# Kernel tuning notes

Measured on AMD Instinct MI355X. Metric: run time of the kernel, lower is better.

## Reference

```python
import jax, jax.numpy as jnp
import numpy as np

HEADS, K = 8, 7

def setup_inputs() -> dict:
    key = jax.random.key(0)
    ks = jax.random.split(key, 8)
    C = 432
    B, H, W = 1, 56, 56
    n = lambda k, s, std: jax.random.normal(k, s, dtype=jnp.float32) * std
    return {
        "x": n(ks[0], (B, H, W, C), 1.0),
        "qkv_w": n(ks[1], (3 * C, C), 0.02),
        "qkv_b": jnp.zeros((3 * C,), jnp.float32),
        "rpb": n(ks[2], (HEADS, 2 * K - 1, 2 * K - 1), 0.02),
        "conv1_w": n(ks[3], (C, C // 54, K, K), 0.05),   # grouped conv, groups=54 -> 8 in-ch per group
        "conv1_b": jnp.zeros((C,), jnp.float32),
        "conv2_w": n(ks[4], (K * K * HEADS, C, 1, 1), 0.05),
        "conv2_b": jnp.zeros((K * K * HEADS,), jnp.float32),
        "ghost_head": n(ks[5], (C, K, K), 0.02),
        "proj2_w": n(ks[6], (C, 2 * C), 0.02),
        "proj2_b": jnp.zeros((C,), jnp.float32),
    }

def _nat_indices(L, K):
    i = jnp.arange(L)
    ni = jnp.clip(i - K // 2, 0, L - K)                      # clamped window start (NAT semantics)
    idx = ni[:, None] + jnp.arange(K)[None, :]               # [L,K] neighbor coords
    rpb_idx = (K - 1) - (i - ni)[:, None] + jnp.arange(K)[None, :]  # [L,K] rpb lookup
    return idx, rpb_idx

def reference(x, qkv_w, qkv_b, rpb, conv1_w, conv1_b, conv2_w, conv2_b, ghost_head, proj2_w, proj2_b):
    B, H, W, C = x.shape
    hd = C // HEADS
    scale = hd ** -0.5
    qkv = (x @ qkv_w.T + qkv_b).reshape(B, H, W, 3, HEADS, hd)
    qkv = jnp.transpose(qkv, (3, 0, 4, 1, 2, 5))             # [3,B,heads,H,W,hd]
    q, k, v = qkv[0], qkv[1], qkv[2]
    q = q * scale
    idx_i, rpb_i = _nat_indices(H, K)
    idx_j, rpb_j = _nat_indices(W, K)
    ii = idx_i[:, None, :, None]                             # [H,1,K,1]
    jj = idx_j[None, :, None, :]                             # [1,W,1,K]
    # ---- NAT QK + RPB ----
    k_nbr = k[:, :, ii, jj, :]                               # [B,heads,H,W,K,K,hd]
    attn = jnp.einsum('bghwd,bghwuvd->bghwuv', q, k_nbr)
    bias = rpb[:, rpb_i[:, None, :, None], rpb_j[None, :, None, :]]  # [heads,H,W,K,K]
    attn = (attn + bias[None]).reshape(B, HEADS, H, W, K * K)
    attn = jax.nn.softmax(attn, axis=-1)
    # ---- Hadamard conv-attention branch ----
    to_nchw = lambda t: jnp.transpose(t, (0, 2, 3, 1, 4)).reshape(B, H, W, C).transpose(0, 3, 1, 2)
    had = to_nchw(q) * to_nchw(k) * scale                    # note: q already scaled once (faithful)
    h = jax.lax.conv_general_dilated(had, conv1_w, (1, 1), ((K // 2, K // 2), (K // 2, K // 2)),
                                     feature_group_count=54,
                                     dimension_numbers=('NCHW', 'OIHW', 'NCHW')) + conv1_b[None, :, None, None]
    h = jax.nn.gelu(h, approximate=False)
    h = jax.lax.conv_general_dilated(h, conv2_w, (1, 1), ((0, 0), (0, 0)),
                                     dimension_numbers=('NCHW', 'OIHW', 'NCHW')) + conv2_b[None, :, None, None]
    h = jax.nn.softmax(h, axis=1)                            # softmax over all heads*K*K channels
    h_attn = jnp.transpose(h, (0, 2, 3, 1)).reshape(B, H, W, HEADS, K * K).transpose(0, 3, 1, 2, 4)
    attn_A = jnp.concatenate([attn, h_attn], axis=-1)        # [B,heads,H,W,2*K*K]
    # ---- ELSA ghost-head local aggregation (zero-padded centered window, lam=0, gamma=1) ----
    v_tmp = to_nchw(v)                                       # [B,C,H,W]
    a_tmp = jnp.transpose(attn_A, (0, 2, 3, 1, 4)).reshape(B, H, W, -1).transpose(0, 3, 1, 2)
    G = 2 * HEADS                                            # 2*K*K slots per head -> 2*heads attn groups
    a_g = a_tmp.reshape(B, G, K * K, H, W)
    vp = jnp.pad(v_tmp, ((0, 0), (0, 0), (K // 2, K // 2), (K // 2, K // 2)))
    pi = jnp.arange(H)[:, None] + jnp.arange(K)[None, :]     # [H,K]
    pj = jnp.arange(W)[:, None] + jnp.arange(K)[None, :]
    patches = vp[:, :, pi[:, None, :, None], pj[None, :, None, :]].reshape(B, C, H, W, K * K)
    elsa = jnp.einsum('bgchwk,bgkhw->bgchw',
                      patches.reshape(B, G, C // G, H, W, K * K), a_g).reshape(B, C, H, W)
    elsa = elsa + jnp.einsum('bchwk,ck->bchw', patches, ghost_head.reshape(C, K * K))
    attn_tmp = jnp.transpose(elsa, (0, 2, 3, 1)).reshape(B, H, W, HEADS, hd).transpose(0, 3, 1, 2, 4)
    # ---- NAT AV over fused attention (both 49-slot halves share the NAT neighborhood) ----
    a2 = (attn_A[..., :K * K] + attn_A[..., K * K:]).reshape(B, HEADS, H, W, K, K)
    v_nbr = v[:, :, ii, jj, :]                               # [B,heads,H,W,K,K,hd]
    av = jnp.einsum('bghwuv,bghwuvd->bghwd', a2, v_nbr)
    out = jnp.concatenate([av, attn_tmp], axis=-1)           # [B,heads,H,W,2*hd]
    out = jnp.transpose(out, (0, 2, 3, 1, 4)).reshape(B, H, W, 2 * C)
    return out @ proj2_w.T + proj2_b
```

## Files before the change

kernel.cpp:

```cpp
#include <hip/hip_runtime.h>
#include <hip/hip_bf16.h>
#include <math.h>

#define N_PIX 3136
#define NPAD 3200
#define CDIM 432
#define NHEADS 8
#define HD 54
#define KK 49
#define C2 392

typedef __attribute__((ext_vector_type(8))) short bf16x8;
typedef __attribute__((ext_vector_type(4))) float f32x4;
typedef __attribute__((ext_vector_type(8))) unsigned short ushort8;

__device__ __forceinline__ void gload_lds16(const void* g, void* l) {
    __builtin_amdgcn_global_load_lds(
        (const __attribute__((address_space(1))) void*)g,
        (__attribute__((address_space(3))) void*)l, 16, 0, 0);
}

__device__ __forceinline__ unsigned short f2bf(float f) {
    __hip_bfloat16 b = __float2bfloat16(f);
    unsigned short u;
    __builtin_memcpy(&u, &b, 2);
    return u;
}

__device__ __forceinline__ size_t perm_off(int r, int k, int Kp) {
    int p = ((k >> 3) & 7) ^ (r & 7);
    return (size_t)r * Kp + ((k >> 6) << 6) + (p << 3) + (k & 7);
}

__device__ __forceinline__ void convert_body(
    const float* __restrict__ src, __hip_bfloat16* __restrict__ dst,
    int Mlog, int Mpad, int Klog, int Kp, int id)
{
    int chunks = Kp >> 3;
    if (id >= Mpad * chunks) return;
    int r = id / chunks, cb = id % chunks;
    int k0 = cb << 3;
    __hip_bfloat16 vv[8];
    #pragma unroll
    for (int e = 0; e < 8; e++) {
        int k = k0 + e;
        float f = (r < Mlog && k < Klog) ? src[(size_t)r * Klog + k] : 0.f;
        vv[e] = __float2bfloat16(f);
    }
    int p = (cb & 7) ^ (r & 7);
    __hip_bfloat16* d = dst + (size_t)r * Kp + ((cb >> 3) << 6) + (p << 3);
    *(ushort8*)d = *(const ushort8*)vv;
}

__global__ __launch_bounds__(256) void prep_kernel(
    const float* __restrict__ x, const float* __restrict__ qkv_w,
    const float* __restrict__ conv2_w, const float* __restrict__ proj2_w,
    const float* __restrict__ ghost,
    __hip_bfloat16* __restrict__ xb, __hip_bfloat16* __restrict__ qkvwb,
    __hip_bfloat16* __restrict__ c2wb, __hip_bfloat16* __restrict__ p2wb,
    float* __restrict__ ghostT, __hip_bfloat16* __restrict__ qkzero)
{
    int b = blockIdx.x;
    if (b < 83) {
        int id = b * 256 + threadIdx.x;
        if (id < CDIM * KK) {
            int cc = id / KK, t = id % KK;
            ghostT[t * CDIM + cc] = ghost[id];
        }
    } else if (b < 769) {
        convert_body(x, xb, 3136, 3136, 432, 448, (b - 83) * 256 + threadIdx.x);
    } else if (b < 1063) {
        convert_body(qkv_w, qkvwb, 1296, 1344, 432, 448, (b - 769) * 256 + threadIdx.x);
    } else if (b < 1161) {
        convert_body(conv2_w, c2wb, 392, 448, 432, 448, (b - 1063) * 256 + threadIdx.x);
    } else if (b < 1357) {
        convert_body(proj2_w, p2wb, 432, 448, 864, 896, (b - 1161) * 256 + threadIdx.x);
    } else {
        int id = (b - 1357) * 256 + threadIdx.x;
        if (id < 409600) ((ushort8*)qkzero)[id] = (ushort8)0;
    }
}

__global__ __launch_bounds__(256) void gemm_mfma(
    const __hip_bfloat16* __restrict__ A, const __hip_bfloat16* __restrict__ B,
    const float* __restrict__ bias,
    float* __restrict__ O0, float* __restrict__ O1,
    __hip_bfloat16* __restrict__ VB,
    __hip_bfloat16* __restrict__ QB, __hip_bfloat16* __restrict__ KB,
    int Nlog, int Kp, int mode, float qscale, int ldO)
{
    __shared__ __hip_bfloat16 lA[64 * 64];
    __shared__ __hip_bfloat16 lB[64 * 64];
    const int tid = threadIdx.x;
    const int w = tid >> 6, lane = tid & 63;
    const int row0 = blockIdx.y * 64, col0 = blockIdx.x * 64;
    const int wr = (w >> 1) * 32, wc = (w & 1) * 32;
    const int srow = lane >> 3, schk = lane & 7;
    f32x4 acc[2][2] = {};

    for (int k0 = 0; k0 < Kp; k0 += 64) {
        #pragma unroll
        for (int t = 0; t < 2; t++) {
            int lid = w * 2 + t;
            const __hip_bfloat16* ga =
                A + (size_t)(row0 + lid * 8 + srow) * Kp + k0 + schk * 8;
            gload_lds16(ga, &lA[lid * 8 * 64]);
            const __hip_bfloat16* gb =
                B + (size_t)(col0 + lid * 8 + srow) * Kp + k0 + schk * 8;
            gload_lds16(gb, &lB[lid * 8 * 64]);
        }
        __syncthreads();
        #pragma unroll
        for (int ks = 0; ks < 2; ks++) {
            bf16x8 af[2], bfr[2];
            int c = ks * 4 + (lane >> 4);
            #pragma unroll
            for (int mi = 0; mi < 2; mi++) {
                int ra = wr + mi * 16 + (lane & 15);
                af[mi] = *(const bf16x8*)&lA[ra * 64 + ((c ^ (ra & 7)) << 3)];
                int rb = wc + mi * 16 + (lane & 15);
                bfr[mi] = *(const bf16x8*)&lB[rb * 64 + ((c ^ (rb & 7)) << 3)];
            }
            #pragma unroll
            for (int mi = 0; mi < 2; mi++)
                #pragma unroll
                for (int ni = 0; ni < 2; ni++)
                    acc[mi][ni] = __builtin_amdgcn_mfma_f32_16x16x32_bf16(
                        af[mi], bfr[ni], acc[mi][ni], 0, 0, 0);
        }
        __syncthreads();
    }

    #pragma unroll
    for (int mi = 0; mi < 2; mi++) {
        #pragma unroll
        for (int ni = 0; ni < 2; ni++) {
            #pragma unroll
            for (int rr = 0; rr < 4; rr++) {
                int r = row0 + wr + mi * 16 + (lane >> 4) * 4 + rr;
                int cc = col0 + wc + ni * 16 + (lane & 15);
                if (cc >= Nlog) continue;
                float val = acc[mi][ni][rr] + bias[cc];
                if (mode == 0) {
                    int s = cc / CDIM, cch = cc - s * CDIM;
                    int hh = cch / HD, dd = cch - hh * HD;
                    if (s == 0) {
                        float qv = val * qscale;
                        O0[(size_t)r * CDIM + cch] = qv;
                        QB[((size_t)hh * NPAD + r) * 64 + dd] = __float2bfloat16(qv);
                    } else if (s == 1) {
                        O1[(size_t)r * CDIM + cch] = val;
                        KB[((size_t)hh * NPAD + r) * 64 + dd] = __float2bfloat16(val);
                    } else {
                        VB[((size_t)hh * N_PIX + r) * 64 + dd] = __float2bfloat16(val);
                    }
                } else {
                    O0[(size_t)r * ldO + cc] = val;
                }
            }
        }
    }
}

__global__ __launch_bounds__(256) void attn_mfma(
    const __hip_bfloat16* __restrict__ qb, const __hip_bfloat16* __restrict__ kb,
    const float* __restrict__ rpb, float* __restrict__ attn)
{
    __shared__ float Sl[16][404];
    __shared__ float rpb_l[169];
    int bid = blockIdx.x;
    int nb = (bid & 7) * 56 + (bid >> 3);
    int h = nb / 56, i = nb - (nb / 56) * 56;
    int tid = threadIdx.x;
    int w = tid >> 6, lane = tid & 63;
    int l15 = lane & 15, l4 = lane >> 4;
    int ni = min(max(i - 3, 0), 49);

    for (int f = tid; f < 169; f += 256) rpb_l[f] = rpb[h * 169 + f];
    __syncthreads();

    const __hip_bfloat16* qrow = qb + ((size_t)h * NPAD + i * 56) * 64;
    const __hip_bfloat16* kwin = kb + ((size_t)h * NPAD + ni * 56) * 64;

    for (int rt = 0; rt < 4; rt++) {
        bf16x8 af0 = *(const bf16x8*)(qrow + (size_t)(rt * 16 + l15) * 64 + l4 * 8);
        bf16x8 af1 = *(const bf16x8*)(qrow + (size_t)(rt * 16 + l15) * 64 + 32 + l4 * 8);
        for (int ct = w; ct < 25; ct += 4) {
            bf16x8 b0 = *(const bf16x8*)(kwin + (size_t)(ct * 16 + l15) * 64 + l4 * 8);
            bf16x8 b1 = *(const bf16x8*)(kwin + (size_t)(ct * 16 + l15) * 64 + 32 + l4 * 8);
            f32x4 acc = {};
            acc = __builtin_amdgcn_mfma_f32_16x16x32_bf16(af0, b0, acc, 0, 0, 0);
            acc = __builtin_amdgcn_mfma_f32_16x16x32_bf16(af1, b1, acc, 0, 0, 0);
            int col = ct * 16 + l15;
            #pragma unroll
            for (int r = 0; r < 4; r++)
                Sl[l4 * 4 + r][col] = acc[r];
        }
        __syncthreads();
        #pragma unroll
        for (int pp = 0; pp < 4; pp++) {
            int j = rt * 16 + w * 4 + pp;
            if (j < 56) {
                int n = i * 56 + j;
                int nj = min(max(j - 3, 0), 49);
                int t = lane;
                float logit = -1e30f;
                if (t < KK) {
                    int u = t / 7, v = t - (t / 7) * 7;
                    int col = u * 56 + nj + v;
                    int ri = 6 - (i - ni) + u;
                    int rj = 6 - (j - nj) + v;
                    logit = Sl[j - rt * 16][col] + rpb_l[ri * 13 + rj];
                }
                float m = logit;
                #pragma unroll
                for (int off = 32; off; off >>= 1) m = fmaxf(m, __shfl_xor(m, off));
                float e = (t < KK) ? expf(logit - m) : 0.f;
                float ssum = e;
                #pragma unroll
                for (int off = 32; off; off >>= 1) ssum += __shfl_xor(ssum, off);
                if (t < KK) attn[(size_t)n * C2 + h * KK + t] = e / ssum;
            }
        }
        __syncthreads();
    }
}

#define TH 4
__global__ __launch_bounds__(256) void conv1_gelu_v2(
    const float* __restrict__ q, const float* __restrict__ k,
    const float* __restrict__ w, const float* __restrict__ b,
    __hip_bfloat16* __restrict__ out, float scale)
{
    int g = blockIdx.x % 54;
    int rt = blockIdx.x / 54;
    int r0 = rt * TH;
    int tid = threadIdx.x;
    int waveid = tid >> 6, lane = tid & 63;
    int ic = lane >> 3, oc = lane & 7;

    __shared__ float smem[10][8][68];

    float* sflat = &smem[0][0][0];
    for (int i = tid; i < 10 * 8 * 68; i += 256) sflat[i] = 0.f;

    float wreg[49];
    {
        const float* wp = w + ((size_t)(g * 8 + oc) * 8 + ic) * 49;
        #pragma unroll
        for (int t = 0; t < 49; t++) wreg[t] = wp[t];
    }
    __syncthreads();

    {
        int lic = tid & 7;
        int lpj = (tid >> 3) & 31;
        for (int rr = 0; rr < 10; rr++) {
            int pi = r0 - 3 + rr;
            if (pi < 0 || pi >= 56) continue;
            #pragma unroll
            for (int p0 = 0; p0 < 56; p0 += 32) {
                int pj = p0 + lpj;
                if (pj < 56) {
                    size_t off = (size_t)(pi * 56 + pj) * CDIM + g * 8 + lic;
                    smem[rr][lic][pj + 3] = q[off] * k[off] * scale;
                }
            }
        }
    }
    __syncthreads();

    int r = r0 + waveid;
    float bias_o = b[g * 8 + oc];
    for (int j0 = 0; j0 < 56; j0 += 4) {
        float acc0 = 0.f, acc1 = 0.f, acc2 = 0.f, acc3 = 0.f;
        #pragma unroll
        for (int u = 0; u < 7; u++) {
            const float* rp = &smem[waveid + u][ic][j0];
            float4 c0 = *(const float4*)(rp);
            float4 c1 = *(const float4*)(rp + 4);
            float4 c2 = *(const float4*)(rp + 8);
            float col[12] = {c0.x, c0.y, c0.z, c0.w,
                             c1.x, c1.y, c1.z, c1.w,
                             c2.x, c2.y, c2.z, c2.w};
            #pragma unroll
            for (int v = 0; v < 7; v++) {
                float wv = wreg[u * 7 + v];
                acc0 += wv * col[v + 0];
                acc1 += wv * col[v + 1];
                acc2 += wv * col[v + 2];
                acc3 += wv * col[v + 3];
            }
        }
        float accs[4] = {acc0, acc1, acc2, acc3};
        #pragma unroll
        for (int jj = 0; jj < 4; jj++) {
            float s = accs[jj];
            s += __shfl_xor(s, 8);
            s += __shfl_xor(s, 16);
            s += __shfl_xor(s, 32);
            accs[jj] = s;
        }
        if (ic == 0) {
            #pragma unroll
            for (int jj = 0; jj < 4; jj++) {
                float a = accs[jj] + bias_o;
                float gl = 0.5f * a * (1.0f + erff(a * 0.70710678118654752f));
                int n = r * 56 + j0 + jj;
                int kch = g * 8 + oc;
                out[perm_off(n, kch, 448)] = __float2bfloat16(gl);
            }
        }
    }
}

__global__ __launch_bounds__(128) void softmax_pack(
    const float* __restrict__ h2, const float* __restrict__ attn,
    unsigned* __restrict__ pk)
{
    __shared__ float red[128];
    int n = blockIdx.x, tid = threadIdx.x;
    const float* row = h2 + (size_t)n * C2;
    float m = -1e30f;
    float rv[4];
    #pragma unroll
    for (int idx = 0; idx < 4; idx++) {
        int c = tid + idx * 128;
        rv[idx] = (c < C2) ? row[c] : -1e30f;
        m = fmaxf(m, rv[idx]);
    }
    red[tid] = m; __syncthreads();
    for (int s = 64; s; s >>= 1) {
        if (tid < s) red[tid] = fmaxf(red[tid], red[tid + s]);
        __syncthreads();
    }
    m = red[0]; __syncthreads();
    float loc = 0.f;
    #pragma unroll
    for (int idx = 0; idx < 4; idx++) {
        int c = tid + idx * 128;
        if (c < C2) { rv[idx] = expf(rv[idx] - m); loc += rv[idx]; }
    }
    red[tid] = loc; __syncthreads();
    for (int s = 64; s; s >>= 1) {
        if (tid < s) red[tid] += red[tid + s];
        __syncthreads();
    }
    float inv = 1.0f / red[0];
    #pragma unroll
    for (int idx = 0; idx < 4; idx++) {
        int c = tid + idx * 128;
        if (c < C2) {
            float hval = rv[idx] * inv;
            float a = attn[(size_t)n * C2 + c];
            int hh = c / KK, t = c - hh * KK;
            unsigned word = ((unsigned)f2bf(a) << 16) | (unsigned)f2bf(a + hval);
            pk[((size_t)n * 8 + hh) * 52 + t] = word;
        }
    }
}

__global__ __launch_bounds__(256) void combine_int(
    const __hip_bfloat16* __restrict__ vb, const unsigned* __restrict__ pk,
    const float* __restrict__ ghostT, __hip_bfloat16* __restrict__ comb)
{
    __shared__ float gs[KK * HD];
    int bid = blockIdx.x;
    int nb = (bid & 7) * 625 + (bid >> 3);
    int h = (nb * 4) / 2500;
    for (int f = threadIdx.x; f < KK * HD; f += 256) {
        int t = f / HD, dd = f - t * HD;
        gs[f] = ghostT[t * CDIM + h * HD + dd];
    }
    __syncthreads();

    int task = nb * 4 + (threadIdx.x >> 6);
    task = __builtin_amdgcn_readfirstlane(task);
    int lane = threadIdx.x & 63;
    int rem = task - h * 2500;
    int i = 3 + rem / 50;
    int j = 3 + (rem - (rem / 50) * 50);
    int n = i * 56 + j;
    int d = (lane < HD) ? lane : (HD - 1);
    bool lo = (d < 27);

    const unsigned* pkrow = pk + ((size_t)n * 8 + h) * 52;
    const __hip_bfloat16* vwin =
        vb + ((size_t)h * N_PIX + (i - 3) * 56 + (j - 3)) * 64 + d;

    float S_ah = 0.f, S_a = 0.f, S_g = 0.f;
    #pragma unroll
    for (int u = 0; u < 7; u++) {
        float vrow[7];
        #pragma unroll
        for (int vv = 0; vv < 7; vv++)
            vrow[vv] = __bfloat162float(vwin[(u * 56 + vv) * 64]);
        #pragma unroll
        for (int vv = 0; vv < 7; vv++) {
            const int t = u * 7 + vv;
            unsigned s = pkrow[t];
            float a  = __uint_as_float(s & 0xFFFF0000u);
            float ah = __uint_as_float(s << 16);
            float gt = gs[t * HD + d];
            S_ah += ah * vrow[vv];
            S_a  += a  * vrow[vv];
            S_g  += gt * vrow[vv];
        }
    }
    if (lane < HD) {
        float av = S_ah;
        float Sh = S_ah - S_a;
        float elsa = S_g + (lo ? S_a : Sh);
        comb[perm_off(n, h * 108 + d, 896)]      = __float2bfloat16(av);
        comb[perm_off(n, h * 108 + 54 + d, 896)] = __float2bfloat16(elsa);
    }
}

__global__ __launch_bounds__(256) void combine_bdr(
    const __hip_bfloat16* __restrict__ vb, const unsigned* __restrict__ pk,
    const float* __restrict__ ghostT, __hip_bfloat16* __restrict__ comb)
{
    __shared__ float gs[KK * HD];
    int bid = blockIdx.x;
    int nb = (bid & 7) * 159 + (bid >> 3);
    int h = (nb * 4) / 636;
    for (int f = threadIdx.x; f < KK * HD; f += 256) {
        int t = f / HD, dd = f - t * HD;
        gs[f] = ghostT[t * CDIM + h * HD + dd];
    }
    __syncthreads();

    int task = nb * 4 + (threadIdx.x >> 6);
    task = __builtin_amdgcn_readfirstlane(task);
    int lane = threadIdx.x & 63;
    int idx = task - h * 636;
    int i, j;
    if (idx < 336) {
        int r = idx / 56;
        i = (r < 3) ? r : 50 + r;
        j = idx - r * 56;
    } else {
        int idx2 = idx - 336;
        i = 3 + idx2 / 6;
        int jj = idx2 - (idx2 / 6) * 6;
        j = (jj < 3) ? jj : 50 + jj;
    }
    int n = i * 56 + j;
    int d = (lane < HD) ? lane : (HD - 1);
    bool lo = (d < 27);

    const unsigned* pkrow = pk + ((size_t)n * 8 + h) * 52;
    int ni = min(max(i - 3, 0), 49), nj = min(max(j - 3, 0), 49);
    const __hip_bfloat16* vhead = vb + (size_t)h * N_PIX * 64 + d;
    const __hip_bfloat16* vbc = vhead + (size_t)(ni * 56 + nj) * 64;

    float S_ahc = 0.f, S_ap = 0.f, S_ahp = 0.f, S_gp = 0.f;
    #pragma unroll
    for (int t = 0; t < KK; t++) {
        const int u = t / 7, vv = t % 7;
        unsigned s = pkrow[t];
        float a  = __uint_as_float(s & 0xFFFF0000u);
        float ah = __uint_as_float(s << 16);
        float vc = __bfloat162float(vbc[(u * 56 + vv) * 64]);
        S_ahc += ah * vc;
        int pi = i + u - 3, pj = j + vv - 3;
        if (pi >= 0 && pi < 56 && pj >= 0 && pj < 56) {
            float vp = __bfloat162float(vhead[(size_t)(pi * 56 + pj) * 64]);
            float gt = gs[t * HD + d];
            S_ahp += ah * vp; S_ap += a * vp; S_gp += gt * vp;
        }
    }
    if (lane < HD) {
        float av = S_ahc;
        float Shp = S_ahp - S_ap;
        float elsa = S_gp + (lo ? S_ap : Shp);
        comb[perm_off(n, h * 108 + d, 896)]      = __float2bfloat16(av);
        comb[perm_off(n, h * 108 + 54 + d, 896)] = __float2bfloat16(elsa);
    }
}

extern "C" void kernel_launch(void* const* d_in, const int* in_sizes, int n_in,
                              void* d_out, int out_size, void* d_ws, size_t ws_size,
                              hipStream_t stream)
{
    const float* x       = (const float*)d_in[0];
    const float* qkv_w   = (const float*)d_in[1];
    const float* qkv_b   = (const float*)d_in[2];
    const float* rpb     = (const float*)d_in[3];
    const float* conv1_w = (const float*)d_in[4];
    const float* conv1_b = (const float*)d_in[5];
    const float* conv2_w = (const float*)d_in[6];
    const float* conv2_b = (const float*)d_in[7];
    const float* ghost   = (const float*)d_in[8];
    const float* proj2_w = (const float*)d_in[9];
    const float* proj2_b = (const float*)d_in[10];
    float* out = (float*)d_out;

    float* ws = (float*)d_ws;
    const size_t NC = (size_t)N_PIX * CDIM;
    const size_t NA = (size_t)N_PIX * C2;
    float* q      = ws;
    float* k      = q + NC;
    float* attn   = k + NC;
    float* hat    = attn + NA;
    float* ghostT = hat + NA;
    unsigned* pk  = (unsigned*)(ghostT + 21168);
    __hip_bfloat16* bfbase = (__hip_bfloat16*)(pk + 1304576);
    __hip_bfloat16* xb     = bfbase;
    __hip_bfloat16* qkvwb  = xb    + (size_t)3136 * 448;
    __hip_bfloat16* c2wb   = qkvwb + (size_t)1344 * 448;
    __hip_bfloat16* p2wb   = c2wb  + (size_t)448 * 448;
    __hip_bfloat16* hb     = p2wb  + (size_t)448 * 896;
    __hip_bfloat16* cb     = hb    + (size_t)3136 * 448;
    __hip_bfloat16* vb16   = cb    + (size_t)3136 * 896;
    __hip_bfloat16* qb16   = vb16  + (size_t)8 * N_PIX * 64;
    __hip_bfloat16* kb16   = qb16  + (size_t)8 * NPAD * 64;

    const float scale = 0.13608276348795434f;

    prep_kernel<<<2957, 256, 0, stream>>>(
        x, qkv_w, conv2_w, proj2_w, ghost, xb, qkvwb, c2wb, p2wb, ghostT, qb16);

    gemm_mfma<<<dim3(21, 49), 256, 0, stream>>>(
        xb, qkvwb, qkv_b, q, k, vb16, qb16, kb16, 1296, 448, 0, scale, 0);

    attn_mfma<<<448, 256, 0, stream>>>(qb16, kb16, rpb, attn);

    conv1_gelu_v2<<<54 * 14, 256, 0, stream>>>(q, k, conv1_w, conv1_b, hb, scale);

    gemm_mfma<<<dim3(7, 49), 256, 0, stream>>>(
        hb, c2wb, conv2_b, hat, nullptr, nullptr, nullptr, nullptr,
        392, 448, 1, 1.f, 392);

    softmax_pack<<<N_PIX, 128, 0, stream>>>(hat, attn, pk);

    combine_int<<<5000, 256, 0, stream>>>(vb16, pk, ghostT, cb);
    combine_bdr<<<1272, 256, 0, stream>>>(vb16, pk, ghostT, cb);

    gemm_mfma<<<dim3(7, 49), 256, 0, stream>>>(
        cb, p2wb, proj2_b, out, nullptr, nullptr, nullptr, nullptr,
        432, 896, 1, 1.f, 432);
}
```

Measured before the change: 151.2 us.

## Use 128x128 GEMM tiles, zero only Q/K pad columns, vectorize conv staging

The MFMA GEMM tile is raised from 64x64 to 128x128 per block. Each wave now computes a 64x64 sub-tile with 4x4 accumulators, and a row bound check is added for the M edge. The prep kernel no longer zeroes the whole bf16 Q/K buffers; it clears only the padding head-dim columns 54..63, which shrinks its grid. The conv1 staging loop switches to float4 loads of q and k. The larger tiles cut global and LDS traffic per FLOP, but the conv2 and proj GEMMs drop to about 100 blocks, which can leave CUs idle. Edge tiles also read past logical rows into neighbouring buffers.

```diff
diff --git a/kernel.cpp b/kernel.cpp
--- a/kernel.cpp
+++ b/kernel.cpp
@@ -13,6 +13,7 @@
 typedef __attribute__((ext_vector_type(8))) short bf16x8;
 typedef __attribute__((ext_vector_type(4))) float f32x4;
 typedef __attribute__((ext_vector_type(8))) unsigned short ushort8;
+typedef __attribute__((ext_vector_type(2))) unsigned short ushort2v;
 
 __device__ __forceinline__ void gload_lds16(const void* g, void* l) {
     __builtin_amdgcn_global_load_lds(
@@ -58,7 +59,7 @@
     const float* __restrict__ ghost,
     __hip_bfloat16* __restrict__ xb, __hip_bfloat16* __restrict__ qkvwb,
     __hip_bfloat16* __restrict__ c2wb, __hip_bfloat16* __restrict__ p2wb,
-    float* __restrict__ ghostT, __hip_bfloat16* __restrict__ qkzero)
+    float* __restrict__ ghostT, __hip_bfloat16* __restrict__ qkbase)
 {
     int b = blockIdx.x;
     if (b < 83) {
@@ -77,31 +78,35 @@
         convert_body(proj2_w, p2wb, 432, 448, 864, 896, (b - 1161) * 256 + threadIdx.x);
     } else {
         int id = (b - 1357) * 256 + threadIdx.x;
-        if (id < 409600) ((ushort8*)qkzero)[id] = (ushort8)0;
-    }
-}
-
-__global__ __launch_bounds__(256) void gemm_mfma(
+        if (id < 2 * 8 * NPAD) {
+            __hip_bfloat16* p = qkbase + (size_t)id * 64;
+            *(ushort2v*)((unsigned short*)p + 54) = (ushort2v)0;
+            *(ushort8*)((unsigned short*)p + 56) = (ushort8)0;
+        }
+    }
+}
+
+__global__ __launch_bounds__(256) void gemm_mfma2(
     const __hip_bfloat16* __restrict__ A, const __hip_bfloat16* __restrict__ B,
     const float* __restrict__ bias,
     float* __restrict__ O0, float* __restrict__ O1,
     __hip_bfloat16* __restrict__ VB,
     __hip_bfloat16* __restrict__ QB, __hip_bfloat16* __restrict__ KB,
-    int Nlog, int Kp, int mode, float qscale, int ldO)
-{
-    __shared__ __hip_bfloat16 lA[64 * 64];
-    __shared__ __hip_bfloat16 lB[64 * 64];
+    int Mlog, int Nlog, int Kp, int mode, float qscale, int ldO)
+{
+    __shared__ __hip_bfloat16 lA[128 * 64];
+    __shared__ __hip_bfloat16 lB[128 * 64];
     const int tid = threadIdx.x;
     const int w = tid >> 6, lane = tid & 63;
-    const int row0 = blockIdx.y * 64, col0 = blockIdx.x * 64;
-    const int wr = (w >> 1) * 32, wc = (w & 1) * 32;
+    const int row0 = blockIdx.y * 128, col0 = blockIdx.x * 128;
+    const int wr = (w >> 1) * 64, wc = (w & 1) * 64;
     const int srow = lane >> 3, schk = lane & 7;
-    f32x4 acc[2][2] = {};
+    f32x4 acc[4][4] = {};
 
     for (int k0 = 0; k0 < Kp; k0 += 64) {
         #pragma unroll
-        for (int t = 0; t < 2; t++) {
-            int lid = w * 2 + t;
+        for (int t = 0; t < 4; t++) {
+            int lid = w * 4 + t;
             const __hip_bfloat16* ga =
                 A + (size_t)(row0 + lid * 8 + srow) * Kp + k0 + schk * 8;
             gload_lds16(ga, &lA[lid * 8 * 64]);
@@ -112,19 +117,19 @@
         __syncthreads();
         #pragma unroll
         for (int ks = 0; ks < 2; ks++) {
-            bf16x8 af[2], bfr[2];
+            bf16x8 af[4], bfr[4];
             int c = ks * 4 + (lane >> 4);
             #pragma unroll
-            for (int mi = 0; mi < 2; mi++) {
+            for (int mi = 0; mi < 4; mi++) {
                 int ra = wr + mi * 16 + (lane & 15);
                 af[mi] = *(const bf16x8*)&lA[ra * 64 + ((c ^ (ra & 7)) << 3)];
                 int rb = wc + mi * 16 + (lane & 15);
                 bfr[mi] = *(const bf16x8*)&lB[rb * 64 + ((c ^ (rb & 7)) << 3)];
             }
             #pragma unroll
-            for (int mi = 0; mi < 2; mi++)
+            for (int mi = 0; mi < 4; mi++)
                 #pragma unroll
-                for (int ni = 0; ni < 2; ni++)
+                for (int ni = 0; ni < 4; ni++)
                     acc[mi][ni] = __builtin_amdgcn_mfma_f32_16x16x32_bf16(
                         af[mi], bfr[ni], acc[mi][ni], 0, 0, 0);
         }
@@ -132,14 +137,14 @@
     }
 
     #pragma unroll
-    for (int mi = 0; mi < 2; mi++) {
-        #pragma unroll
-        for (int ni = 0; ni < 2; ni++) {
+    for (int mi = 0; mi < 4; mi++) {
+        #pragma unroll
+        for (int ni = 0; ni < 4; ni++) {
             #pragma unroll
             for (int rr = 0; rr < 4; rr++) {
                 int r = row0 + wr + mi * 16 + (lane >> 4) * 4 + rr;
                 int cc = col0 + wc + ni * 16 + (lane & 15);
-                if (cc >= Nlog) continue;
+                if (r >= Mlog || cc >= Nlog) continue;
                 float val = acc[mi][ni][rr] + bias[cc];
                 if (mode == 0) {
                     int s = cc / CDIM, cch = cc - s * CDIM;
@@ -252,20 +257,19 @@
     }
     __syncthreads();
 
-    {
-        int lic = tid & 7;
-        int lpj = (tid >> 3) & 31;
-        for (int rr = 0; rr < 10; rr++) {
-            int pi = r0 - 3 + rr;
-            if (pi < 0 || pi >= 56) continue;
-            #pragma unroll
-            for (int p0 = 0; p0 < 56; p0 += 32) {
-                int pj = p0 + lpj;
-                if (pj < 56) {
-                    size_t off = (size_t)(pi * 56 + pj) * CDIM + g * 8 + lic;
-                    smem[rr][lic][pj + 3] = q[off] * k[off] * scale;
-                }
-            }
+    for (int f = tid; f < 10 * 56 * 2; f += 256) {
+        int rr = f / 112, rem = f - rr * 112;
+        int pj = rem >> 1, half = rem & 1;
+        int pi = r0 - 3 + rr;
+        if (pi >= 0 && pi < 56) {
+            size_t off = (size_t)(pi * 56 + pj) * CDIM + g * 8 + half * 4;
+            float4 qv = *(const float4*)(q + off);
+            float4 kv = *(const float4*)(k + off);
+            int c0 = half * 4;
+            smem[rr][c0 + 0][pj + 3] = qv.x * kv.x * scale;
+            smem[rr][c0 + 1][pj + 3] = qv.y * kv.y * scale;
+            smem[rr][c0 + 2][pj + 3] = qv.z * kv.z * scale;
+            smem[rr][c0 + 3][pj + 3] = qv.w * kv.w * scale;
         }
     }
     __syncthreads();
@@ -518,26 +522,26 @@
 
     const float scale = 0.13608276348795434f;
 
-    prep_kernel<<<2957, 256, 0, stream>>>(
+    prep_kernel<<<1557, 256, 0, stream>>>(
         x, qkv_w, conv2_w, proj2_w, ghost, xb, qkvwb, c2wb, p2wb, ghostT, qb16);
 
-    gemm_mfma<<<dim3(21, 49), 256, 0, stream>>>(
-        xb, qkvwb, qkv_b, q, k, vb16, qb16, kb16, 1296, 448, 0, scale, 0);
+    gemm_mfma2<<<dim3(11, 25), 256, 0, stream>>>(
+        xb, qkvwb, qkv_b, q, k, vb16, qb16, kb16, 3136, 1296, 448, 0, scale, 0);
 
     attn_mfma<<<448, 256, 0, stream>>>(qb16, kb16, rpb, attn);
 
     conv1_gelu_v2<<<54 * 14, 256, 0, stream>>>(q, k, conv1_w, conv1_b, hb, scale);
 
-    gemm_mfma<<<dim3(7, 49), 256, 0, stream>>>(
+    gemm_mfma2<<<dim3(4, 25), 256, 0, stream>>>(
         hb, c2wb, conv2_b, hat, nullptr, nullptr, nullptr, nullptr,
-        392, 448, 1, 1.f, 392);
+        3136, 392, 448, 1, 1.f, 392);
 
     softmax_pack<<<N_PIX, 128, 0, stream>>>(hat, attn, pk);
 
     combine_int<<<5000, 256, 0, stream>>>(vb16, pk, ghostT, cb);
     combine_bdr<<<1272, 256, 0, stream>>>(vb16, pk, ghostT, cb);
 
-    gemm_mfma<<<dim3(7, 49), 256, 0, stream>>>(
+    gemm_mfma2<<<dim3(4, 25), 256, 0, stream>>>(
         cb, p2wb, proj2_b, out, nullptr, nullptr, nullptr, nullptr,
-        432, 896, 1, 1.f, 432);
-}
+        3136, 432, 896, 1, 1.f, 432);
+}
```

After: 184.5 us. +22.1%, slower.

## Merge independent kernels into shared launches and trim padding zero-fill

Applied to the files above, without the earlier changes.

Combines attention-logit/softmax and the grouped conv1+GELU kernels into one launch whose block index picks the branch. Does the same for the interior and border combine kernels. The prep kernel now zeroes only the padded tail columns (54..63) of the Q/K bf16 buffers instead of the whole buffer, and conv1 loads q/k with float4 vector loads. The aim is to cut launch overhead and tail idle time and let independent work overlap. In exchange, shared memory is sized to the larger branch, which may lower occupancy for the smaller branch.

```diff
diff --git a/kernel.cpp b/kernel.cpp
--- a/kernel.cpp
+++ b/kernel.cpp
@@ -13,6 +13,7 @@
 typedef __attribute__((ext_vector_type(8))) short bf16x8;
 typedef __attribute__((ext_vector_type(4))) float f32x4;
 typedef __attribute__((ext_vector_type(8))) unsigned short ushort8;
+typedef __attribute__((ext_vector_type(2))) unsigned short ushort2v;
 
 __device__ __forceinline__ void gload_lds16(const void* g, void* l) {
     __builtin_amdgcn_global_load_lds(
@@ -58,7 +59,7 @@
     const float* __restrict__ ghost,
     __hip_bfloat16* __restrict__ xb, __hip_bfloat16* __restrict__ qkvwb,
     __hip_bfloat16* __restrict__ c2wb, __hip_bfloat16* __restrict__ p2wb,
-    float* __restrict__ ghostT, __hip_bfloat16* __restrict__ qkzero)
+    float* __restrict__ ghostT, __hip_bfloat16* __restrict__ qkbase)
 {
     int b = blockIdx.x;
     if (b < 83) {
@@ -77,7 +78,11 @@
         convert_body(proj2_w, p2wb, 432, 448, 864, 896, (b - 1161) * 256 + threadIdx.x);
     } else {
         int id = (b - 1357) * 256 + threadIdx.x;
-        if (id < 409600) ((ushort8*)qkzero)[id] = (ushort8)0;
+        if (id < 2 * 8 * NPAD) {
+            __hip_bfloat16* p = qkbase + (size_t)id * 64;
+            *(ushort2v*)((unsigned short*)p + 54) = (ushort2v)0;
+            *(ushort8*)((unsigned short*)p + 56) = (ushort8)0;
+        }
     }
 }
 
@@ -162,153 +167,152 @@
     }
 }
 
-__global__ __launch_bounds__(256) void attn_mfma(
+#define TH 4
+__global__ __launch_bounds__(256) void attn_conv1(
     const __hip_bfloat16* __restrict__ qb, const __hip_bfloat16* __restrict__ kb,
-    const float* __restrict__ rpb, float* __restrict__ attn)
-{
-    __shared__ float Sl[16][404];
-    __shared__ float rpb_l[169];
-    int bid = blockIdx.x;
-    int nb = (bid & 7) * 56 + (bid >> 3);
-    int h = nb / 56, i = nb - (nb / 56) * 56;
-    int tid = threadIdx.x;
-    int w = tid >> 6, lane = tid & 63;
-    int l15 = lane & 15, l4 = lane >> 4;
-    int ni = min(max(i - 3, 0), 49);
-
-    for (int f = tid; f < 169; f += 256) rpb_l[f] = rpb[h * 169 + f];
-    __syncthreads();
-
-    const __hip_bfloat16* qrow = qb + ((size_t)h * NPAD + i * 56) * 64;
-    const __hip_bfloat16* kwin = kb + ((size_t)h * NPAD + ni * 56) * 64;
-
-    for (int rt = 0; rt < 4; rt++) {
-        bf16x8 af0 = *(const bf16x8*)(qrow + (size_t)(rt * 16 + l15) * 64 + l4 * 8);
-        bf16x8 af1 = *(const bf16x8*)(qrow + (size_t)(rt * 16 + l15) * 64 + 32 + l4 * 8);
-        for (int ct = w; ct < 25; ct += 4) {
-            bf16x8 b0 = *(const bf16x8*)(kwin + (size_t)(ct * 16 + l15) * 64 + l4 * 8);
-            bf16x8 b1 = *(const bf16x8*)(kwin + (size_t)(ct * 16 + l15) * 64 + 32 + l4 * 8);
-            f32x4 acc = {};
-            acc = __builtin_amdgcn_mfma_f32_16x16x32_bf16(af0, b0, acc, 0, 0, 0);
-            acc = __builtin_amdgcn_mfma_f32_16x16x32_bf16(af1, b1, acc, 0, 0, 0);
-            int col = ct * 16 + l15;
-            #pragma unroll
-            for (int r = 0; r < 4; r++)
-                Sl[l4 * 4 + r][col] = acc[r];
-        }
-        __syncthreads();
-        #pragma unroll
-        for (int pp = 0; pp < 4; pp++) {
-            int j = rt * 16 + w * 4 + pp;
-            if (j < 56) {
-                int n = i * 56 + j;
-                int nj = min(max(j - 3, 0), 49);
-                int t = lane;
-                float logit = -1e30f;
-                if (t < KK) {
-                    int u = t / 7, v = t - (t / 7) * 7;
-                    int col = u * 56 + nj + v;
-                    int ri = 6 - (i - ni) + u;
-                    int rj = 6 - (j - nj) + v;
-                    logit = Sl[j - rt * 16][col] + rpb_l[ri * 13 + rj];
-                }
-                float m = logit;
-                #pragma unroll
-                for (int off = 32; off; off >>= 1) m = fmaxf(m, __shfl_xor(m, off));
-                float e = (t < KK) ? expf(logit - m) : 0.f;
-                float ssum = e;
-                #pragma unroll
-                for (int off = 32; off; off >>= 1) ssum += __shfl_xor(ssum, off);
-                if (t < KK) attn[(size_t)n * C2 + h * KK + t] = e / ssum;
-            }
-        }
-        __syncthreads();
-    }
-}
-
-#define TH 4
-__global__ __launch_bounds__(256) void conv1_gelu_v2(
+    const float* __restrict__ rpb, float* __restrict__ attn,
     const float* __restrict__ q, const float* __restrict__ k,
     const float* __restrict__ w, const float* __restrict__ b,
     __hip_bfloat16* __restrict__ out, float scale)
 {
-    int g = blockIdx.x % 54;
-    int rt = blockIdx.x / 54;
-    int r0 = rt * TH;
+    __shared__ char sraw[26536];
     int tid = threadIdx.x;
-    int waveid = tid >> 6, lane = tid & 63;
-    int ic = lane >> 3, oc = lane & 7;
-
-    __shared__ float smem[10][8][68];
-
-    float* sflat = &smem[0][0][0];
-    for (int i = tid; i < 10 * 8 * 68; i += 256) sflat[i] = 0.f;
-
-    float wreg[49];
-    {
-        const float* wp = w + ((size_t)(g * 8 + oc) * 8 + ic) * 49;
-        #pragma unroll
-        for (int t = 0; t < 49; t++) wreg[t] = wp[t];
-    }
-    __syncthreads();
-
-    {
-        int lic = tid & 7;
-        int lpj = (tid >> 3) & 31;
-        for (int rr = 0; rr < 10; rr++) {
+
+    if (blockIdx.x < 448) {
+        float (*Sl)[404] = (float(*)[404])sraw;
+        float* rpb_l = (float*)(sraw + 16 * 404 * 4);
+        int bid = blockIdx.x;
+        int nb = (bid & 7) * 56 + (bid >> 3);
+        int h = nb / 56, i = nb - (nb / 56) * 56;
+        int wv = tid >> 6, lane = tid & 63;
+        int l15 = lane & 15, l4 = lane >> 4;
+        int ni = min(max(i - 3, 0), 49);
+
+        for (int f = tid; f < 169; f += 256) rpb_l[f] = rpb[h * 169 + f];
+        __syncthreads();
+
+        const __hip_bfloat16* qrow = qb + ((size_t)h * NPAD + i * 56) * 64;
+        const __hip_bfloat16* kwin = kb + ((size_t)h * NPAD + ni * 56) * 64;
+
+        for (int rt = 0; rt < 4; rt++) {
+            bf16x8 af0 = *(const bf16x8*)(qrow + (size_t)(rt * 16 + l15) * 64 + l4 * 8);
+            bf16x8 af1 = *(const bf16x8*)(qrow + (size_t)(rt * 16 + l15) * 64 + 32 + l4 * 8);
+            for (int ct = wv; ct < 25; ct += 4) {
+                bf16x8 b0 = *(const bf16x8*)(kwin + (size_t)(ct * 16 + l15) * 64 + l4 * 8);
+                bf16x8 b1 = *(const bf16x8*)(kwin + (size_t)(ct * 16 + l15) * 64 + 32 + l4 * 8);
+                f32x4 acc = {};
+                acc = __builtin_amdgcn_mfma_f32_16x16x32_bf16(af0, b0, acc, 0, 0, 0);
+                acc = __builtin_amdgcn_mfma_f32_16x16x32_bf16(af1, b1, acc, 0, 0, 0);
+                int col = ct * 16 + l15;
+                #pragma unroll
+                for (int r = 0; r < 4; r++)
+                    Sl[l4 * 4 + r][col] = acc[r];
+            }
+            __syncthreads();
+            #pragma unroll
+            for (int pp = 0; pp < 4; pp++) {
+                int j = rt * 16 + wv * 4 + pp;
+                if (j < 56) {
+                    int n = i * 56 + j;
+                    int nj = min(max(j - 3, 0), 49);
+                    int t = lane;
+                    float logit = -1e30f;
+                    if (t < KK) {
+                        int u = t / 7, v = t - (t / 7) * 7;
+                        int col = u * 56 + nj + v;
+                        int ri = 6 - (i - ni) + u;
+                        int rj = 6 - (j - nj) + v;
+                        logit = Sl[j - rt * 16][col] + rpb_l[ri * 13 + rj];
+                    }
+                    float m = logit;
+                    #pragma unroll
+                    for (int off = 32; off; off >>= 1) m = fmaxf(m, __shfl_xor(m, off));
+                    float e = (t < KK) ? expf(logit - m) : 0.f;
+                    float ssum = e;
+                    #pragma unroll
+                    for (int off = 32; off; off >>= 1) ssum += __shfl_xor(ssum, off);
+                    if (t < KK) attn[(size_t)n * C2 + h * KK + t] = e / ssum;
+                }
+            }
+            __syncthreads();
+        }
+    } else {
+        float (*smem)[8][68] = (float(*)[8][68])sraw;
+        int cb = blockIdx.x - 448;
+        int g = cb % 54;
+        int rt = cb / 54;
+        int r0 = rt * TH;
+        int waveid = tid >> 6, lane = tid & 63;
+        int ic = lane >> 3, oc = lane & 7;
+
+        float* sflat = &smem[0][0][0];
+        for (int i = tid; i < 10 * 8 * 68; i += 256) sflat[i] = 0.f;
+
+        float wreg[49];
+        {
+            const float* wp = w + ((size_t)(g * 8 + oc) * 8 + ic) * 49;
+            #pragma unroll
+            for (int t = 0; t < 49; t++) wreg[t] = wp[t];
+        }
+        __syncthreads();
+
+        for (int f = tid; f < 10 * 56 * 2; f += 256) {
+            int rr = f / 112, rem = f - rr * 112;
+            int pj = rem >> 1, half = rem & 1;
             int pi = r0 - 3 + rr;
-            if (pi < 0 || pi >= 56) continue;
-            #pragma unroll
-            for (int p0 = 0; p0 < 56; p0 += 32) {
-                int pj = p0 + lpj;
-                if (pj < 56) {
-                    size_t off = (size_t)(pi * 56 + pj) * CDIM + g * 8 + lic;
-                    smem[rr][lic][pj + 3] = q[off] * k[off] * scale;
+            if (pi >= 0 && pi < 56) {
+                size_t off = (size_t)(pi * 56 + pj) * CDIM + g * 8 + half * 4;
+                float4 qv = *(const float4*)(q + off);
+                float4 kv = *(const float4*)(k + off);
+                int c0 = half * 4;
+                smem[rr][c0 + 0][pj + 3] = qv.x * kv.x * scale;
+                smem[rr][c0 + 1][pj + 3] = qv.y * kv.y * scale;
+                smem[rr][c0 + 2][pj + 3] = qv.z * kv.z * scale;
+                smem[rr][c0 + 3][pj + 3] = qv.w * kv.w * scale;
+            }
+        }
+        __syncthreads();
+
+        int r = r0 + waveid;
+        float bias_o = b[g * 8 + oc];
+        for (int j0 = 0; j0 < 56; j0 += 4) {
+            float acc0 = 0.f, acc1 = 0.f, acc2 = 0.f, acc3 = 0.f;
+            #pragma unroll
+            for (int u = 0; u < 7; u++) {
+                const float* rp = &smem[waveid + u][ic][j0];
+                float4 c0 = *(const float4*)(rp);
+                float4 c1 = *(const float4*)(rp + 4);
+                float4 c2 = *(const float4*)(rp + 8);
+                float col[12] = {c0.x, c0.y, c0.z, c0.w,
+                                 c1.x, c1.y, c1.z, c1.w,
+                                 c2.x, c2.y, c2.z, c2.w};
+                #pragma unroll
+                for (int v = 0; v < 7; v++) {
+                    float wv2 = wreg[u * 7 + v];
+                    acc0 += wv2 * col[v + 0];
+                    acc1 += wv2 * col[v + 1];
+                    acc2 += wv2 * col[v + 2];
+                    acc3 += wv2 * col[v + 3];
                 }
             }
-        }
-    }
-    __syncthreads();
-
-    int r = r0 + waveid;
-    float bias_o = b[g * 8 + oc];
-    for (int j0 = 0; j0 < 56; j0 += 4) {
-        float acc0 = 0.f, acc1 = 0.f, acc2 = 0.f, acc3 = 0.f;
-        #pragma unroll
-        for (int u = 0; u < 7; u++) {
-            const float* rp = &smem[waveid + u][ic][j0];
-            float4 c0 = *(const float4*)(rp);
-            float4 c1 = *(const float4*)(rp + 4);
-            float4 c2 = *(const float4*)(rp + 8);
-            float col[12] = {c0.x, c0.y, c0.z, c0.w,
-                             c1.x, c1.y, c1.z, c1.w,
-                             c2.x, c2.y, c2.z, c2.w};
-            #pragma unroll
-            for (int v = 0; v < 7; v++) {
-                float wv = wreg[u * 7 + v];
-                acc0 += wv * col[v + 0];
-                acc1 += wv * col[v + 1];
-                acc2 += wv * col[v + 2];
-                acc3 += wv * col[v + 3];
-            }
-        }
-        float accs[4] = {acc0, acc1, acc2, acc3};
-        #pragma unroll
-        for (int jj = 0; jj < 4; jj++) {
-            float s = accs[jj];
-            s += __shfl_xor(s, 8);
-            s += __shfl_xor(s, 16);
-            s += __shfl_xor(s, 32);
-            accs[jj] = s;
-        }
-        if (ic == 0) {
+            float accs[4] = {acc0, acc1, acc2, acc3};
             #pragma unroll
             for (int jj = 0; jj < 4; jj++) {
-                float a = accs[jj] + bias_o;
-                float gl = 0.5f * a * (1.0f + erff(a * 0.70710678118654752f));
-                int n = r * 56 + j0 + jj;
-                int kch = g * 8 + oc;
-                out[perm_off(n, kch, 448)] = __float2bfloat16(gl);
+                float s = accs[jj];
+                s += __shfl_xor(s, 8);
+                s += __shfl_xor(s, 16);
+                s += __shfl_xor(s, 32);
+                accs[jj] = s;
+            }
+            if (ic == 0) {
+                #pragma unroll
+                for (int jj = 0; jj < 4; jj++) {
+                    float a = accs[jj] + bias_o;
+                    float gl = 0.5f * a * (1.0f + erff(a * 0.70710678118654752f));
+                    int n = r * 56 + j0 + jj;
+                    int kch = g * 8 + oc;
+                    out[perm_off(n, kch, 448)] = __float2bfloat16(gl);
+                }
             }
         }
     }
@@ -360,122 +364,119 @@
     }
 }
 
-__global__ __launch_bounds__(256) void combine_int(
+__global__ __launch_bounds__(256) void combine_fused(
     const __hip_bfloat16* __restrict__ vb, const unsigned* __restrict__ pk,
     const float* __restrict__ ghostT, __hip_bfloat16* __restrict__ comb)
 {
     __shared__ float gs[KK * HD];
-    int bid = blockIdx.x;
-    int nb = (bid & 7) * 625 + (bid >> 3);
-    int h = (nb * 4) / 2500;
-    for (int f = threadIdx.x; f < KK * HD; f += 256) {
-        int t = f / HD, dd = f - t * HD;
-        gs[f] = ghostT[t * CDIM + h * HD + dd];
-    }
-    __syncthreads();
-
-    int task = nb * 4 + (threadIdx.x >> 6);
-    task = __builtin_amdgcn_readfirstlane(task);
-    int lane = threadIdx.x & 63;
-    int rem = task - h * 2500;
-    int i = 3 + rem / 50;
-    int j = 3 + (rem - (rem / 50) * 50);
-    int n = i * 56 + j;
-    int d = (lane < HD) ? lane : (HD - 1);
-    bool lo = (d < 27);
-
-    const unsigned* pkrow = pk + ((size_t)n * 8 + h) * 52;
-    const __hip_bfloat16* vwin =
-        vb + ((size_t)h * N_PIX + (i - 3) * 56 + (j - 3)) * 64 + d;
-
-    float S_ah = 0.f, S_a = 0.f, S_g = 0.f;
-    #pragma unroll
-    for (int u = 0; u < 7; u++) {
-        float vrow[7];
+    int tid = threadIdx.x;
+    int lane = tid & 63;
+
+    if (blockIdx.x < 5000) {
+        int bid = blockIdx.x;
+        int nb = (bid & 7) * 625 + (bid >> 3);
+        int h = (nb * 4) / 2500;
+        for (int f = tid; f < KK * HD; f += 256) {
+            int t = f / HD, dd = f - t * HD;
+            gs[f] = ghostT[t * CDIM + h * HD + dd];
+        }
+        __syncthreads();
+
+        int task = nb * 4 + (tid >> 6);
+        task = __builtin_amdgcn_readfirstlane(task);
+        int rem = task - h * 2500;
+        int i = 3 + rem / 50;
+        int j = 3 + (rem - (rem / 50) * 50);
+        int n = i * 56 + j;
+        int d = (lane < HD) ? lane : (HD - 1);
+        bool lo = (d < 27);
+
+        const unsigned* pkrow = pk + ((size_t)n * 8 + h) * 52;
+        const __hip_bfloat16* vwin =
+            vb + ((size_t)h * N_PIX + (i - 3) * 56 + (j - 3)) * 64 + d;
+
+        float S_ah = 0.f, S_a = 0.f, S_g = 0.f;
         #pragma unroll
-        for (int vv = 0; vv < 7; vv++)
-            vrow[vv] = __bfloat162float(vwin[(u * 56 + vv) * 64]);
+        for (int u = 0; u < 7; u++) {
+            float vrow[7];
+            #pragma unroll
+            for (int vv = 0; vv < 7; vv++)
+                vrow[vv] = __bfloat162float(vwin[(u * 56 + vv) * 64]);
+            #pragma unroll
+            for (int vv = 0; vv < 7; vv++) {
+                const int t = u * 7 + vv;
+                unsigned s = pkrow[t];
+                float a  = __uint_as_float(s & 0xFFFF0000u);
+                float ah = __uint_as_float(s << 16);
+                float gt = gs[t * HD + d];
+                S_ah += ah * vrow[vv];
+                S_a  += a  * vrow[vv];
+                S_g  += gt * vrow[vv];
+            }
+        }
+        if (lane < HD) {
+            float av = S_ah;
+            float Sh = S_ah - S_a;
+            float elsa = S_g + (lo ? S_a : Sh);
+            comb[perm_off(n, h * 108 + d, 896)]      = __float2bfloat16(av);
+            comb[perm_off(n, h * 108 + 54 + d, 896)] = __float2bfloat16(elsa);
+        }
+    } else {
+        int bid = blockIdx.x - 5000;
+        int nb = (bid & 7) * 159 + (bid >> 3);
+        int h = (nb * 4) / 636;
+        for (int f = tid; f < KK * HD; f += 256) {
+            int t = f / HD, dd = f - t * HD;
+            gs[f] = ghostT[t * CDIM + h * HD + dd];
+        }
+        __syncthreads();
+
+        int task = nb * 4 + (tid >> 6);
+        task = __builtin_amdgcn_readfirstlane(task);
+        int idx = task - h * 636;
+        int i, j;
+        if (idx < 336) {
+            int r = idx / 56;
+            i = (r < 3) ? r : 50 + r;
+            j = idx - r * 56;
+        } else {
+            int idx2 = idx - 336;
+            i = 3 + idx2 / 6;
+            int jj = idx2 - (idx2 / 6) * 6;
+            j = (jj < 3) ? jj : 50 + jj;
+        }
+        int n = i * 56 + j;
+        int d = (lane < HD) ? lane : (HD - 1);
+        bool lo = (d < 27);
+
+        const unsigned* pkrow = pk + ((size_t)n * 8 + h) * 52;
+        int ni = min(max(i - 3, 0), 49), nj = min(max(j - 3, 0), 49);
+        const __hip_bfloat16* vhead = vb + (size_t)h * N_PIX * 64 + d;
+        const __hip_bfloat16* vbc = vhead + (size_t)(ni * 56 + nj) * 64;
+
+        float S_ahc = 0.f, S_ap = 0.f, S_ahp = 0.f, S_gp = 0.f;
         #pragma unroll
-        for (int vv = 0; vv < 7; vv++) {
-            const int t = u * 7 + vv;
+        for (int t = 0; t < KK; t++) {
+            const int u = t / 7, vv = t % 7;
             unsigned s = pkrow[t];
             float a  = __uint_as_float(s & 0xFFFF0000u);
             float ah = __uint_as_float(s << 16);
-            float gt = gs[t * HD + d];
-            S_ah += ah * vrow[vv];
-            S_a  += a  * vrow[vv];
-            S_g  += gt * vrow[vv];
-        }
-    }
-    if (lane < HD) {
-        float av = S_ah;
-        float Sh = S_ah - S_a;
-        float elsa = S_g + (lo ? S_a : Sh);
-        comb[perm_off(n, h * 108 + d, 896)]      = __float2bfloat16(av);
-        comb[perm_off(n, h * 108 + 54 + d, 896)] = __float2bfloat16(elsa);
-    }
-}
-
-__global__ __launch_bounds__(256) void combine_bdr(
-    const __hip_bfloat16* __restrict__ vb, const unsigned* __restrict__ pk,
-    const float* __restrict__ ghostT, __hip_bfloat16* __restrict__ comb)
-{
-    __shared__ float gs[KK * HD];
-    int bid = blockIdx.x;
-    int nb = (bid & 7) * 159 + (bid >> 3);
-    int h = (nb * 4) / 636;
-    for (int f = threadIdx.x; f < KK * HD; f += 256) {
-        int t = f / HD, dd = f - t * HD;
-        gs[f] = ghostT[t * CDIM + h * HD + dd];
-    }
-    __syncthreads();
-
-    int task = nb * 4 + (threadIdx.x >> 6);
-    task = __builtin_amdgcn_readfirstlane(task);
-    int lane = threadIdx.x & 63;
-    int idx = task - h * 636;
-    int i, j;
-    if (idx < 336) {
-        int r = idx / 56;
-        i = (r < 3) ? r : 50 + r;
-        j = idx - r * 56;
-    } else {
-        int idx2 = idx - 336;
-        i = 3 + idx2 / 6;
-        int jj = idx2 - (idx2 / 6) * 6;
-        j = (jj < 3) ? jj : 50 + jj;
-    }
-    int n = i * 56 + j;
-    int d = (lane < HD) ? lane : (HD - 1);
-    bool lo = (d < 27);
-
-    const unsigned* pkrow = pk + ((size_t)n * 8 + h) * 52;
-    int ni = min(max(i - 3, 0), 49), nj = min(max(j - 3, 0), 49);
-    const __hip_bfloat16* vhead = vb + (size_t)h * N_PIX * 64 + d;
-    const __hip_bfloat16* vbc = vhead + (size_t)(ni * 56 + nj) * 64;
-
-    float S_ahc = 0.f, S_ap = 0.f, S_ahp = 0.f, S_gp = 0.f;
-    #pragma unroll
-    for (int t = 0; t < KK; t++) {
-        const int u = t / 7, vv = t % 7;
-        unsigned s = pkrow[t];
-        float a  = __uint_as_float(s & 0xFFFF0000u);
-        float ah = __uint_as_float(s << 16);
-        float vc = __bfloat162float(vbc[(u * 56 + vv) * 64]);
-        S_ahc += ah * vc;
-        int pi = i + u - 3, pj = j + vv - 3;
-        if (pi >= 0 && pi < 56 && pj >= 0 && pj < 56) {
-            float vp = __bfloat162float(vhead[(size_t)(pi * 56 + pj) * 64]);
-            float gt = gs[t * HD + d];
-            S_ahp += ah * vp; S_ap += a * vp; S_gp += gt * vp;
-        }
-    }
-    if (lane < HD) {
-        float av = S_ahc;
-        float Shp = S_ahp - S_ap;
-        float elsa = S_gp + (lo ? S_ap : Shp);
-        comb[perm_off(n, h * 108 + d, 896)]      = __float2bfloat16(av);
-        comb[perm_off(n, h * 108 + 54 + d, 896)] = __float2bfloat16(elsa);
+            float vc = __bfloat162float(vbc[(u * 56 + vv) * 64]);
+            S_ahc += ah * vc;
+            int pi = i + u - 3, pj = j + vv - 3;
+            if (pi >= 0 && pi < 56 && pj >= 0 && pj < 56) {
+                float vp = __bfloat162float(vhead[(size_t)(pi * 56 + pj) * 64]);
+                float gt = gs[t * HD + d];
+                S_ahp += ah * vp; S_ap += a * vp; S_gp += gt * vp;
+            }
+        }
+        if (lane < HD) {
+            float av = S_ahc;
+            float Shp = S_ahp - S_ap;
+            float elsa = S_gp + (lo ? S_ap : Shp);
+            comb[perm_off(n, h * 108 + d, 896)]      = __float2bfloat16(av);
+            comb[perm_off(n, h * 108 + 54 + d, 896)] = __float2bfloat16(elsa);
+        }
     }
 }
 
@@ -518,15 +519,14 @@
 
     const float scale = 0.13608276348795434f;
 
-    prep_kernel<<<2957, 256, 0, stream>>>(
+    prep_kernel<<<1557, 256, 0, stream>>>(
         x, qkv_w, conv2_w, proj2_w, ghost, xb, qkvwb, c2wb, p2wb, ghostT, qb16);
 
     gemm_mfma<<<dim3(21, 49), 256, 0, stream>>>(
         xb, qkvwb, qkv_b, q, k, vb16, qb16, kb16, 1296, 448, 0, scale, 0);
 
-    attn_mfma<<<448, 256, 0, stream>>>(qb16, kb16, rpb, attn);
-
-    conv1_gelu_v2<<<54 * 14, 256, 0, stream>>>(q, k, conv1_w, conv1_b, hb, scale);
+    attn_conv1<<<448 + 756, 256, 0, stream>>>(
+        qb16, kb16, rpb, attn, q, k, conv1_w, conv1_b, hb, scale);
 
     gemm_mfma<<<dim3(7, 49), 256, 0, stream>>>(
         hb, c2wb, conv2_b, hat, nullptr, nullptr, nullptr, nullptr,
@@ -534,8 +534,7 @@
 
     softmax_pack<<<N_PIX, 128, 0, stream>>>(hat, attn, pk);
 
-    combine_int<<<5000, 256, 0, stream>>>(vb16, pk, ghostT, cb);
-    combine_bdr<<<1272, 256, 0, stream>>>(vb16, pk, ghostT, cb);
+    combine_fused<<<5000 + 1272, 256, 0, stream>>>(vb16, pk, ghostT, cb);
 
     gemm_mfma<<<dim3(7, 49), 256, 0, stream>>>(
         cb, p2wb, proj2_b, out, nullptr, nullptr, nullptr, nullptr,
```

Result: faster. 126.1 us, median of 2 (-16.6%).
